# Optimization experiments

Measured on AMD Instinct MI355X. Metric: run time of the kernel, lower is better.

Reference implementation:

```python
import jax, jax.numpy as jnp
import numpy as np

B, S, D, H = 2, 2048, 1024, 16
DK = D // H
EPS = 1e-5


def setup_inputs() -> dict:
    key = jax.random.key(0)
    ks = jax.random.split(key, 12)
    s = 1.0 / np.sqrt(D)
    return {
        "q": jax.random.normal(ks[0], (B, S, D), dtype=jnp.float32),
        "k": jax.random.normal(ks[1], (B, S, D), dtype=jnp.float32),
        "v": jax.random.normal(ks[2], (B, S, D), dtype=jnp.float32),
        "mask": jnp.ones((B, S, S), dtype=jnp.int32),
        "Wq": jax.random.normal(ks[3], (D, D), dtype=jnp.float32) * s,
        "bq": jnp.zeros((D,), dtype=jnp.float32),
        "Wk": jax.random.normal(ks[4], (D, D), dtype=jnp.float32) * s,
        "bk": jnp.zeros((D,), dtype=jnp.float32),
        "Wv": jax.random.normal(ks[5], (D, D), dtype=jnp.float32) * s,
        "bv": jnp.zeros((D,), dtype=jnp.float32),
        "Wo": jax.random.normal(ks[6], (D, D), dtype=jnp.float32) * s,
        "bo": jnp.zeros((D,), dtype=jnp.float32),
        "gamma": jnp.ones((D,), dtype=jnp.float32),
        "beta": jnp.zeros((D,), dtype=jnp.float32),
    }


def _split_heads(x):
    # [B,S,D] -> [B,H,S,DK]
    return x.reshape(B, S, H, DK).transpose(0, 2, 1, 3)


def reference(q, k, v, mask, Wq, bq, Wk, bk, Wv, bv, Wo, bo, gamma, beta):
    residual = q
    qh = _split_heads(q @ Wq.T + bq)
    kh = _split_heads(k @ Wk.T + bk)
    vh = _split_heads(v @ Wv.T + bv)
    scale = 1.0 / jnp.sqrt(jnp.float32(DK))
    scores = jnp.einsum("bhqd,bhkd->bhqk", qh, kh) * scale
    scores = jnp.where(mask[:, None, :, :] == 0, jnp.float32(-1e9), scores)
    attention = jax.nn.softmax(scores, axis=-1)  # dropout is identity at eval
    ctx = jnp.einsum("bhqk,bhkd->bhqd", attention, vh)
    ctx = ctx.transpose(0, 2, 1, 3).reshape(B, S, D)
    out = ctx @ Wo.T + bo  # output dropout identity at eval
    x = out + residual
    mu = jnp.mean(x, axis=-1, keepdims=True)
    var = jnp.mean((x - mu) ** 2, axis=-1, keepdims=True)
    out = (x - mu) * jax.lax.rsqrt(var + EPS) * gamma + beta
    return out, attention
```

## Files before the change

kernel.cpp:

```cpp
#include <hip/hip_runtime.h>
#include <math.h>

#define B_ 2
#define S_ 2048
#define D_ 1024
#define H_ 16
#define DK_ 64
#define EPS_ 1e-5f

typedef __bf16 bf16_t;
typedef __bf16 bf16x4 __attribute__((ext_vector_type(4)));
typedef __bf16 bf16x8 __attribute__((ext_vector_type(8)));
typedef float f32x4 __attribute__((ext_vector_type(4)));
typedef unsigned long long u64;
typedef unsigned short u16;

#define MFMA16(a, b, c) __builtin_amdgcn_mfma_f32_16x16x32_bf16(a, b, c, 0, 0, 0)

__device__ __forceinline__ void gload16(const bf16_t* g, bf16_t* l) {
    __builtin_amdgcn_global_load_lds(
        (const __attribute__((address_space(1))) void*)g,
        (__attribute__((address_space(3))) void*)l, 16, 0, 0);
}

__global__ __launch_bounds__(256) void cvt3(const float* __restrict__ a,
        const float* __restrict__ b, const float* __restrict__ c,
        bf16_t* __restrict__ oa, bf16_t* __restrict__ ob, bf16_t* __restrict__ oc)
{
    int region = blockIdx.x >> 11;
    int i = ((blockIdx.x & 2047) << 8) + threadIdx.x;
    const float* in = (region == 0) ? a : (region == 1) ? b : c;
    bf16_t* out = (region == 0) ? oa : (region == 1) ? ob : oc;
    float4 v0 = reinterpret_cast<const float4*>(in)[i * 2];
    float4 v1 = reinterpret_cast<const float4*>(in)[i * 2 + 1];
    bf16x8 o = { (bf16_t)v0.x, (bf16_t)v0.y, (bf16_t)v0.z, (bf16_t)v0.w,
                 (bf16_t)v1.x, (bf16_t)v1.y, (bf16_t)v1.z, (bf16_t)v1.w };
    reinterpret_cast<bf16x8*>(out)[i] = o;
}

__global__ __launch_bounds__(256) void cvt4(const float* __restrict__ a,
        const float* __restrict__ b, const float* __restrict__ c, const float* __restrict__ d,
        bf16_t* __restrict__ oa, bf16_t* __restrict__ ob, bf16_t* __restrict__ oc,
        bf16_t* __restrict__ od)
{
    int region = blockIdx.x >> 9;
    int i = ((blockIdx.x & 511) << 8) + threadIdx.x;
    const float* in = (region == 0) ? a : (region == 1) ? b : (region == 2) ? c : d;
    bf16_t* out = (region == 0) ? oa : (region == 1) ? ob : (region == 2) ? oc : od;
    float4 v0 = reinterpret_cast<const float4*>(in)[i * 2];
    float4 v1 = reinterpret_cast<const float4*>(in)[i * 2 + 1];
    bf16x8 o = { (bf16_t)v0.x, (bf16_t)v0.y, (bf16_t)v0.z, (bf16_t)v0.w,
                 (bf16_t)v1.x, (bf16_t)v1.y, (bf16_t)v1.z, (bf16_t)v1.w };
    reinterpret_cast<bf16x8*>(out)[i] = o;
}

__global__ __launch_bounds__(256) void mask_pack(const int* __restrict__ mask,
                                                 u16* __restrict__ bits2)
{
    size_t i = (size_t)blockIdx.x * 256 + threadIdx.x;
    int m = mask[i];
    u64 wm = __ballot(m != 0);
    if ((threadIdx.x & 63) == 0) {
        size_t widx = i >> 6;
        size_t row = widx >> 5;
        int t = (int)(widx & 31);
#pragma unroll
        for (int g = 0; g < 4; ++g) {
            u16 v = 0;
#pragma unroll
            for (int tk = 0; tk < 4; ++tk)
                v |= (u16)(((wm >> (tk * 16 + g * 4)) & 0xF) << (tk * 4));
            bits2[(row * 4 + g) * 32 + t] = v;
        }
    }
}

__device__ __forceinline__ void gemm_body(
        const bf16_t* __restrict__ Asrc, const bf16_t* __restrict__ Bsrc,
        const float* __restrict__ bias, const float* __restrict__ resid,
        float* __restrict__ xout, bf16_t* __restrict__ bout,
        int mode, int m0, int n0)
{
    __shared__ bf16_t As[128 * 64];
    __shared__ bf16_t Bs[128 * 64];
    const int tid = threadIdx.x;
    const int w = tid >> 6, l = tid & 63;
    const int c = l & 15, g = l >> 4;
    const int wr = w >> 1, wc = w & 1;

    int srow[4], scol[4];
    uint32_t soff[4];
#pragma unroll
    for (int i = 0; i < 4; ++i) {
        int s = tid + i * 256;
        srow[i] = s >> 3;
        scol[i] = s & 7;
        soff[i] = (uint32_t)(s * 16) ^ (uint32_t)((srow[i] & 7) << 4);
    }

    bf16x8 areg[4], breg[4];
#pragma unroll
    for (int i = 0; i < 4; ++i) {
        areg[i] = *reinterpret_cast<const bf16x8*>(Asrc + (size_t)srow[i] * D_ + scol[i] * 8);
        breg[i] = *reinterpret_cast<const bf16x8*>(Bsrc + (size_t)srow[i] * D_ + scol[i] * 8);
    }

    f32x4 acc[4][4] = {};
    for (int kt = 0; kt < 16; ++kt) {
#pragma unroll
        for (int i = 0; i < 4; ++i) {
            *reinterpret_cast<bf16x8*>((char*)As + soff[i]) = areg[i];
            *reinterpret_cast<bf16x8*>((char*)Bs + soff[i]) = breg[i];
        }
        __syncthreads();
        if (kt + 1 < 16) {
            int k0 = (kt + 1) * 64;
#pragma unroll
            for (int i = 0; i < 4; ++i) {
                areg[i] = *reinterpret_cast<const bf16x8*>(Asrc + (size_t)srow[i] * D_ + k0 + scol[i] * 8);
                breg[i] = *reinterpret_cast<const bf16x8*>(Bsrc + (size_t)srow[i] * D_ + k0 + scol[i] * 8);
            }
        }
        bf16x8 bf0[4], bf1[4];
#pragma unroll
        for (int j = 0; j < 4; ++j) {
            int R = wc * 64 + j * 16 + c;
            const char* base = (const char*)Bs + R * 128;
            uint32_t msk = (uint32_t)((R & 7) << 4);
            bf0[j] = *reinterpret_cast<const bf16x8*>(base + ((g * 16) ^ msk));
            bf1[j] = *reinterpret_cast<const bf16x8*>(base + ((64 + g * 16) ^ msk));
        }
#pragma unroll
        for (int i = 0; i < 4; ++i) {
            int R = wr * 64 + i * 16 + c;
            const char* base = (const char*)As + R * 128;
            uint32_t msk = (uint32_t)((R & 7) << 4);
            bf16x8 a0 = *reinterpret_cast<const bf16x8*>(base + ((g * 16) ^ msk));
            bf16x8 a1 = *reinterpret_cast<const bf16x8*>(base + ((64 + g * 16) ^ msk));
#pragma unroll
            for (int j = 0; j < 4; ++j) {
                acc[i][j] = MFMA16(a0, bf0[j], acc[i][j]);
                acc[i][j] = MFMA16(a1, bf1[j], acc[i][j]);
            }
        }
        __syncthreads();
    }

#pragma unroll
    for (int i = 0; i < 4; ++i) {
#pragma unroll
        for (int j = 0; j < 4; ++j) {
#pragma unroll
            for (int r = 0; r < 4; ++r) {
                int P  = wr * 64 + i * 16 + g * 4 + r;
                int Qd = wc * 64 + j * 16 + c;
                float val = acc[i][j][r];
                if (mode == 2) {
                    int m = m0 + P, n = n0 + Qd;
                    xout[(size_t)m * D_ + n] = val + bias[n] + resid[(size_t)m * D_ + n];
                } else if (mode == 0) {
                    int m = m0 + P, n = n0 + Qd;
                    int bb = m >> 11, s = m & (S_ - 1);
                    int h = n >> 6, dk = n & 63;
                    bout[(((size_t)bb * H_ + h) * S_ + s) * DK_ + dk] = (bf16_t)(val + bias[n]);
                } else {
                    int n = n0 + P, m = m0 + Qd;
                    int bb = m >> 11, s = m & (S_ - 1);
                    int h = n >> 6, dk = n & 63;
                    bout[(((size_t)bb * H_ + h) * DK_ + dk) * S_ + s] = (bf16_t)(val + bias[n]);
                }
            }
        }
    }
}

__global__ __launch_bounds__(256) void qkv_gemm(
        const bf16_t* __restrict__ xq, const bf16_t* __restrict__ xk,
        const bf16_t* __restrict__ xv,
        const bf16_t* __restrict__ wq, const bf16_t* __restrict__ wk,
        const bf16_t* __restrict__ wv,
        const float* __restrict__ bq, const float* __restrict__ bk,
        const float* __restrict__ bv,
        bf16_t* __restrict__ qh, bf16_t* __restrict__ kh, bf16_t* __restrict__ vt)
{
    const int z = blockIdx.z;
    const int m0 = blockIdx.y * 128, n0 = blockIdx.x * 128;
    const bf16_t* X = (z == 0) ? xq : (z == 1) ? xk : xv;
    const bf16_t* W = (z == 0) ? wq : (z == 1) ? wk : wv;
    const float* bias = (z == 0) ? bq : (z == 1) ? bk : bv;
    bf16_t* out = (z == 0) ? qh : (z == 1) ? kh : vt;
    int mode = (z == 2) ? 1 : 0;
    const bf16_t* Asrc = (mode == 1) ? (W + (size_t)n0 * D_) : (X + (size_t)m0 * D_);
    const bf16_t* Bsrc = (mode == 1) ? (X + (size_t)m0 * D_) : (W + (size_t)n0 * D_);
    gemm_body(Asrc, Bsrc, bias, nullptr, nullptr, out, mode, m0, n0);
}

__global__ __launch_bounds__(256) void oproj_gemm(
        const bf16_t* __restrict__ ctx, const bf16_t* __restrict__ wo,
        const float* __restrict__ bo, const float* __restrict__ resid,
        float* __restrict__ x)
{
    const int m0 = blockIdx.y * 128, n0 = blockIdx.x * 128;
    gemm_body(ctx + (size_t)m0 * D_, wo + (size_t)n0 * D_, bo, resid, x, nullptr, 2, m0, n0);
}

__global__ __launch_bounds__(512) void fused_attn(
        const bf16_t* __restrict__ qh,
        const bf16_t* __restrict__ kh,
        const bf16_t* __restrict__ vt,
        const u16*    __restrict__ bits2,
        float* __restrict__ attn,
        bf16_t* __restrict__ ctx)
{
    constexpr int TILE = 64;
    constexpr int NT = S_ / TILE;
    __shared__ bf16_t Kbuf[3][TILE * DK_];
    __shared__ bf16_t Vbuf[3][TILE * DK_];
    __shared__ float  Pf[8][16 * 64];

    const int tid = threadIdx.x;
    const int w = tid >> 6, l = tid & 63;
    const int c = l & 15, g = l >> 4;

    const int id = blockIdx.x;
    const int xcd = id & 7, ixd = id >> 3;
    const int bh = xcd * 4 + (ixd >> 4);
    const int qt = ixd & 15;
    const int q0 = qt * 128 + w * 16;
    const int b = bh >> 4, h = bh & 15;

    const bf16_t* Q = qh + ((size_t)bh * S_ + q0) * DK_;
    const bf16_t* K = kh + (size_t)bh * S_ * DK_;
    const bf16_t* V = vt + (size_t)bh * DK_ * S_;
    float* Astrip = attn + ((size_t)bh * S_ + q0) * S_;

    u64 mreg[8];
    {
        const u64* mp = reinterpret_cast<const u64*>(
            bits2 + (((size_t)b * S_ + q0 + c) * 4 + g) * 32);
#pragma unroll
        for (int i = 0; i < 8; ++i) mreg[i] = mp[i];
    }

    bf16x8 qf0 = *reinterpret_cast<const bf16x8*>(&Q[c * DK_ + g * 8]);
    bf16x8 qf1 = *reinterpret_cast<const bf16x8*>(&Q[c * DK_ + 32 + g * 8]);

    const int row_s = (w << 3) + (l >> 3);
    const int csx = (l & 7) ^ (row_s & 7);
    const bf16_t* Kg = K + (size_t)row_s * DK_ + csx * 8;
    const bf16_t* Vg = V + (size_t)row_s * S_ + csx * 8;
    const int woffu = __builtin_amdgcn_readfirstlane(w * 512);
    const uint32_t rm = (uint32_t)((c & 7) << 4);
    const uint32_t xr = (uint32_t)((c & 7) << 4);

    gload16(Kg, &Kbuf[0][woffu]);
    gload16(Kg + (size_t)TILE * DK_, &Kbuf[1][woffu]);
    asm volatile("s_waitcnt vmcnt(1)" ::: "memory");
    __builtin_amdgcn_s_barrier();

    float l_r = 0.f;
    int bc = 0;
    for (int t = 0; t < NT; ++t) {
        if (t + 2 < NT) {
            int b2 = bc + 2; if (b2 >= 3) b2 -= 3;
            gload16(Kg + (size_t)(t + 2) * TILE * DK_, &Kbuf[b2][woffu]);
        }
        __builtin_amdgcn_sched_barrier(0);
        u16 m16 = (u16)(mreg[t >> 2] >> ((t & 3) << 4));
        const char* kb = (const char*)&Kbuf[bc][0];
        f32x4 acc[4] = {};
        __builtin_amdgcn_s_setprio(1);
#pragma unroll
        for (int tk = 0; tk < 4; ++tk) {
            uint32_t base = (uint32_t)((tk * 16 + c) * 128 + g * 16);
            bf16x8 a0 = *reinterpret_cast<const bf16x8*>(kb + (base ^ rm));
            bf16x8 a1 = *reinterpret_cast<const bf16x8*>(kb + ((base + 64) ^ rm));
            acc[tk] = MFMA16(a0, qf0, acc[tk]);
            acc[tk] = MFMA16(a1, qf1, acc[tk]);
        }
        __builtin_amdgcn_s_setprio(0);
        float ps = 0.f;
#pragma unroll
        for (int tk = 0; tk < 4; ++tk) {
#pragma unroll
            for (int r = 0; r < 4; ++r) {
                float e = __expf(acc[tk][r] * 0.125f);
                e = ((m16 >> (tk * 4 + r)) & 1) ? e : 0.f;
                ps += e;
            }
        }
        l_r += ps;
        if (t + 2 < NT) asm volatile("s_waitcnt vmcnt(1)" ::: "memory");
        else            asm volatile("s_waitcnt vmcnt(0)" ::: "memory");
        asm volatile("s_waitcnt lgkmcnt(0)" ::: "memory");
        __builtin_amdgcn_sched_barrier(0);
        __builtin_amdgcn_s_barrier();
        bc = (bc == 2) ? 0 : bc + 1;
    }
    l_r += __shfl_xor(l_r, 16);
    l_r += __shfl_xor(l_r, 32);
    const float inv_l = 1.0f / l_r;

    gload16(Kg, &Kbuf[0][woffu]);
    gload16(Vg, &Vbuf[0][woffu]);
    gload16(Kg + (size_t)TILE * DK_, &Kbuf[1][woffu]);
    gload16(Vg + TILE, &Vbuf[1][woffu]);
    asm volatile("s_waitcnt vmcnt(2)" ::: "memory");
    __builtin_amdgcn_s_barrier();

    float* pf = &Pf[w][0];
    f32x4 oacc[4] = {};
    bc = 0;
    for (int t = 0; t < NT; ++t) {
        if (t + 2 < NT) {
            int b2 = bc + 2; if (b2 >= 3) b2 -= 3;
            gload16(Kg + (size_t)(t + 2) * TILE * DK_, &Kbuf[b2][woffu]);
            gload16(Vg + (t + 2) * TILE, &Vbuf[b2][woffu]);
        }
        __builtin_amdgcn_sched_barrier(0);
        u16 m16 = (u16)(mreg[t >> 2] >> ((t & 3) << 4));
        const char* kb = (const char*)&Kbuf[bc][0];
        const char* vb = (const char*)&Vbuf[bc][0];
        f32x4 acc[4] = {};
        __builtin_amdgcn_s_setprio(1);
#pragma unroll
        for (int tk = 0; tk < 4; ++tk) {
            uint32_t base = (uint32_t)((tk * 16 + c) * 128 + g * 16);
            bf16x8 a0 = *reinterpret_cast<const bf16x8*>(kb + (base ^ rm));
            bf16x8 a1 = *reinterpret_cast<const bf16x8*>(kb + ((base + 64) ^ rm));
            acc[tk] = MFMA16(a0, qf0, acc[tk]);
            acc[tk] = MFMA16(a1, qf1, acc[tk]);
        }
        __builtin_amdgcn_s_setprio(0);
#pragma unroll
        for (int tk = 0; tk < 4; ++tk) {
            f32x4 pv;
#pragma unroll
            for (int r = 0; r < 4; ++r) {
                float p = __expf(acc[tk][r] * 0.125f) * inv_l;
                pv[r] = ((m16 >> (tk * 4 + r)) & 1) ? p : 0.f;
            }
            *reinterpret_cast<f32x4*>((char*)pf + ((uint32_t)(c * 256 + tk * 64 + g * 16) ^ xr)) = pv;
        }
        asm volatile("s_waitcnt lgkmcnt(0)" ::: "memory");
        __builtin_amdgcn_sched_barrier(0);
#pragma unroll
        for (int i = 0; i < 4; ++i) {
            int row = i * 4 + (l >> 4);
            uint32_t off = (uint32_t)(i * 1024 + l * 16) ^ (uint32_t)((row & 7) << 4);
            f32x4 sv = *reinterpret_cast<const f32x4*>((char*)pf + off);
            __builtin_nontemporal_store(sv,
                reinterpret_cast<f32x4*>(Astrip + (size_t)row * S_ + t * TILE + (l & 15) * 4));
        }
        f32x4 p0a = *reinterpret_cast<const f32x4*>((char*)pf + ((uint32_t)(c * 256 + g * 32) ^ xr));
        f32x4 p0b = *reinterpret_cast<const f32x4*>((char*)pf + ((uint32_t)(c * 256 + g * 32 + 16) ^ xr));
        f32x4 p1a = *reinterpret_cast<const f32x4*>((char*)pf + ((uint32_t)(c * 256 + 128 + g * 32) ^ xr));
        f32x4 p1b = *reinterpret_cast<const f32x4*>((char*)pf + ((uint32_t)(c * 256 + 128 + g * 32 + 16) ^ xr));
        bf16x8 pa0 = { (bf16_t)p0a[0], (bf16_t)p0a[1], (bf16_t)p0a[2], (bf16_t)p0a[3],
                       (bf16_t)p0b[0], (bf16_t)p0b[1], (bf16_t)p0b[2], (bf16_t)p0b[3] };
        bf16x8 pa1 = { (bf16_t)p1a[0], (bf16_t)p1a[1], (bf16_t)p1a[2], (bf16_t)p1a[3],
                       (bf16_t)p1b[0], (bf16_t)p1b[1], (bf16_t)p1b[2], (bf16_t)p1b[3] };
        __builtin_amdgcn_s_setprio(1);
#pragma unroll
        for (int tk = 0; tk < 4; ++tk) {
            uint32_t base = (uint32_t)((tk * 16 + c) * 128 + g * 16);
            bf16x8 b0 = *reinterpret_cast<const bf16x8*>(vb + (base ^ rm));
            bf16x8 b1 = *reinterpret_cast<const bf16x8*>(vb + ((base + 64) ^ rm));
            oacc[tk] = MFMA16(pa0, b0, oacc[tk]);
            oacc[tk] = MFMA16(pa1, b1, oacc[tk]);
        }
        __builtin_amdgcn_s_setprio(0);
        if (t + 2 < NT)       asm volatile("s_waitcnt vmcnt(6)" ::: "memory");
        else if (t + 1 < NT)  asm volatile("s_waitcnt vmcnt(4)" ::: "memory");
        asm volatile("s_waitcnt lgkmcnt(0)" ::: "memory");
        __builtin_amdgcn_sched_barrier(0);
        __builtin_amdgcn_s_barrier();
        bc = (bc == 2) ? 0 : bc + 1;
    }

#pragma unroll
    for (int tk = 0; tk < 4; ++tk) {
#pragma unroll
        for (int r = 0; r < 4; ++r) {
            int q = q0 + g * 4 + r;
            ctx[((size_t)b * S_ + q) * D_ + h * DK_ + tk * 16 + c] = (bf16_t)oacc[tk][r];
        }
    }
}

__global__ void ln_kernel(const float* __restrict__ x, const float* __restrict__ gamma,
                          const float* __restrict__ beta, float* __restrict__ out)
{
    int row = blockIdx.x;
    const float* xr = x + (size_t)row * D_;
    int tid = threadIdx.x;
    float v[4];
    float s = 0.f;
#pragma unroll
    for (int i = 0; i < 4; ++i) {
        v[i] = xr[tid + i * 256];
        s += v[i];
    }
#pragma unroll
    for (int off = 32; off > 0; off >>= 1) s += __shfl_xor(s, off);
    __shared__ float red[4];
    int wid = tid >> 6, lane = tid & 63;
    if (lane == 0) red[wid] = s;
    __syncthreads();
    float mu = (red[0] + red[1] + red[2] + red[3]) * (1.0f / D_);
    float vs = 0.f;
#pragma unroll
    for (int i = 0; i < 4; ++i) {
        float d = v[i] - mu;
        vs += d * d;
    }
#pragma unroll
    for (int off = 32; off > 0; off >>= 1) vs += __shfl_xor(vs, off);
    __syncthreads();
    __shared__ float red2[4];
    if (lane == 0) red2[wid] = vs;
    __syncthreads();
    float var = (red2[0] + red2[1] + red2[2] + red2[3]) * (1.0f / D_);
    float rs = rsqrtf(var + EPS_);
#pragma unroll
    for (int i = 0; i < 4; ++i) {
        int c = tid + i * 256;
        out[(size_t)row * D_ + c] = (v[i] - mu) * rs * gamma[c] + beta[c];
    }
}

extern "C" void kernel_launch(void* const* d_in, const int* in_sizes, int n_in,
                              void* d_out, int out_size, void* d_ws, size_t ws_size,
                              hipStream_t stream) {
    const float* q    = (const float*)d_in[0];
    const float* k    = (const float*)d_in[1];
    const float* v    = (const float*)d_in[2];
    const int*   mask = (const int*)d_in[3];
    const float* Wq   = (const float*)d_in[4];
    const float* bq   = (const float*)d_in[5];
    const float* Wk   = (const float*)d_in[6];
    const float* bk   = (const float*)d_in[7];
    const float* Wv   = (const float*)d_in[8];
    const float* bv   = (const float*)d_in[9];
    const float* Wo   = (const float*)d_in[10];
    const float* bo   = (const float*)d_in[11];
    const float* gamma= (const float*)d_in[12];
    const float* beta = (const float*)d_in[13];

    float* out  = (float*)d_out;
    float* attn = out + (size_t)B_ * S_ * D_;

    uint8_t* ws = (uint8_t*)d_ws;
    bf16_t* xq  = (bf16_t*)(ws);
    bf16_t* xk  = (bf16_t*)(ws + ((size_t)8  << 20));
    bf16_t* xv  = (bf16_t*)(ws + ((size_t)16 << 20));
    bf16_t* wqb = (bf16_t*)(ws + ((size_t)24 << 20));
    bf16_t* wkb = (bf16_t*)(ws + ((size_t)26 << 20));
    bf16_t* wvb = (bf16_t*)(ws + ((size_t)28 << 20));
    bf16_t* wob = (bf16_t*)(ws + ((size_t)30 << 20));
    bf16_t* qh  = (bf16_t*)(ws + ((size_t)32 << 20));
    u16*    bits= (u16*)   (ws + ((size_t)40 << 20));
    bf16_t* kh  = (bf16_t*)(ws + ((size_t)42 << 20));
    bf16_t* vt  = (bf16_t*)(ws + ((size_t)50 << 20));
    bf16_t* ctx = (bf16_t*)(ws);
    float*  x   = (float*) (ws + ((size_t)8 << 20));

    dim3 blk(256);
    cvt3<<<dim3(6144), blk, 0, stream>>>(q, k, v, xq, xk, xv);
    cvt4<<<dim3(2048), blk, 0, stream>>>(Wq, Wk, Wv, Wo, wqb, wkb, wvb, wob);
    mask_pack<<<dim3((B_ * S_ * S_) / 256), blk, 0, stream>>>(mask, bits);

    dim3 gqkv(D_ / 128, (B_ * S_) / 128, 3);
    qkv_gemm<<<gqkv, blk, 0, stream>>>(xq, xk, xv, wqb, wkb, wvb,
                                       bq, bk, bv, qh, kh, vt);

    fused_attn<<<dim3(512), dim3(512), 0, stream>>>(qh, kh, vt, bits, attn, ctx);

    dim3 ggemm(D_ / 128, (B_ * S_) / 128);
    oproj_gemm<<<ggemm, blk, 0, stream>>>(ctx, wob, bo, q, x);
    ln_kernel<<<dim3(B_ * S_), blk, 0, stream>>>(x, gamma, beta, out);
}
```

Measured before the change: 268.7 us.

## Split attention softmax-stats pass into separate kernel and merge prep kernels

The two-pass fused attention kernel is split so that the row-sum (softmax denominator) pass runs in its own kernel, `attn_stats`. That kernel uses 256-thread blocks over 64-query tiles, giving 1024 blocks, and writes inverse sums to a workspace buffer. The emit kernel then reads those sums instead of recomputing them. The aim is more parallelism and occupancy for the stats pass, which used to run inside the 512-block grid. The three conversion and mask-pack launches are also merged into one `prep` kernel to cut launch overhead. The cost is an extra launch, a global round-trip for the sums, and a second read of Q/K.

```diff
diff --git a/kernel.cpp b/kernel.cpp
--- a/kernel.cpp
+++ b/kernel.cpp
@@ -23,55 +23,56 @@
         (__attribute__((address_space(3))) void*)l, 16, 0, 0);
 }
 
-__global__ __launch_bounds__(256) void cvt3(const float* __restrict__ a,
-        const float* __restrict__ b, const float* __restrict__ c,
-        bf16_t* __restrict__ oa, bf16_t* __restrict__ ob, bf16_t* __restrict__ oc)
-{
-    int region = blockIdx.x >> 11;
-    int i = ((blockIdx.x & 2047) << 8) + threadIdx.x;
-    const float* in = (region == 0) ? a : (region == 1) ? b : c;
-    bf16_t* out = (region == 0) ? oa : (region == 1) ? ob : oc;
-    float4 v0 = reinterpret_cast<const float4*>(in)[i * 2];
-    float4 v1 = reinterpret_cast<const float4*>(in)[i * 2 + 1];
-    bf16x8 o = { (bf16_t)v0.x, (bf16_t)v0.y, (bf16_t)v0.z, (bf16_t)v0.w,
-                 (bf16_t)v1.x, (bf16_t)v1.y, (bf16_t)v1.z, (bf16_t)v1.w };
-    reinterpret_cast<bf16x8*>(out)[i] = o;
-}
-
-__global__ __launch_bounds__(256) void cvt4(const float* __restrict__ a,
-        const float* __restrict__ b, const float* __restrict__ c, const float* __restrict__ d,
-        bf16_t* __restrict__ oa, bf16_t* __restrict__ ob, bf16_t* __restrict__ oc,
-        bf16_t* __restrict__ od)
-{
-    int region = blockIdx.x >> 9;
-    int i = ((blockIdx.x & 511) << 8) + threadIdx.x;
-    const float* in = (region == 0) ? a : (region == 1) ? b : (region == 2) ? c : d;
-    bf16_t* out = (region == 0) ? oa : (region == 1) ? ob : (region == 2) ? oc : od;
-    float4 v0 = reinterpret_cast<const float4*>(in)[i * 2];
-    float4 v1 = reinterpret_cast<const float4*>(in)[i * 2 + 1];
-    bf16x8 o = { (bf16_t)v0.x, (bf16_t)v0.y, (bf16_t)v0.z, (bf16_t)v0.w,
-                 (bf16_t)v1.x, (bf16_t)v1.y, (bf16_t)v1.z, (bf16_t)v1.w };
-    reinterpret_cast<bf16x8*>(out)[i] = o;
-}
-
-__global__ __launch_bounds__(256) void mask_pack(const int* __restrict__ mask,
-                                                 u16* __restrict__ bits2)
-{
-    size_t i = (size_t)blockIdx.x * 256 + threadIdx.x;
-    int m = mask[i];
-    u64 wm = __ballot(m != 0);
-    if ((threadIdx.x & 63) == 0) {
-        size_t widx = i >> 6;
-        size_t row = widx >> 5;
-        int t = (int)(widx & 31);
-#pragma unroll
-        for (int g = 0; g < 4; ++g) {
-            u16 v = 0;
-#pragma unroll
-            for (int tk = 0; tk < 4; ++tk)
-                v |= (u16)(((wm >> (tk * 16 + g * 4)) & 0xF) << (tk * 4));
-            bits2[(row * 4 + g) * 32 + t] = v;
-        }
+__global__ __launch_bounds__(256) void prep(
+        const int* __restrict__ mask, u16* __restrict__ bits2,
+        const float* __restrict__ q, const float* __restrict__ k,
+        const float* __restrict__ v,
+        bf16_t* __restrict__ xq, bf16_t* __restrict__ xk, bf16_t* __restrict__ xv,
+        const float* __restrict__ Wq, const float* __restrict__ Wk,
+        const float* __restrict__ Wv, const float* __restrict__ Wo,
+        bf16_t* __restrict__ wq, bf16_t* __restrict__ wk,
+        bf16_t* __restrict__ wv, bf16_t* __restrict__ wo)
+{
+    int bid = blockIdx.x;
+    if (bid < 32768) {
+        size_t i = (size_t)bid * 256 + threadIdx.x;
+        int m = mask[i];
+        u64 wm = __ballot(m != 0);
+        if ((threadIdx.x & 63) == 0) {
+            size_t widx = i >> 6;
+            size_t row = widx >> 5;
+            int t = (int)(widx & 31);
+#pragma unroll
+            for (int g = 0; g < 4; ++g) {
+                u16 val = 0;
+#pragma unroll
+                for (int tk = 0; tk < 4; ++tk)
+                    val |= (u16)(((wm >> (tk * 16 + g * 4)) & 0xF) << (tk * 4));
+                bits2[(row * 4 + g) * 32 + t] = val;
+            }
+        }
+    } else if (bid < 38912) {
+        int b2 = bid - 32768;
+        int region = b2 >> 11;
+        int i = ((b2 & 2047) << 8) + threadIdx.x;
+        const float* in = (region == 0) ? q : (region == 1) ? k : v;
+        bf16_t* out = (region == 0) ? xq : (region == 1) ? xk : xv;
+        float4 v0 = reinterpret_cast<const float4*>(in)[i * 2];
+        float4 v1 = reinterpret_cast<const float4*>(in)[i * 2 + 1];
+        bf16x8 o = { (bf16_t)v0.x, (bf16_t)v0.y, (bf16_t)v0.z, (bf16_t)v0.w,
+                     (bf16_t)v1.x, (bf16_t)v1.y, (bf16_t)v1.z, (bf16_t)v1.w };
+        reinterpret_cast<bf16x8*>(out)[i] = o;
+    } else {
+        int b2 = bid - 38912;
+        int region = b2 >> 9;
+        int i = ((b2 & 511) << 8) + threadIdx.x;
+        const float* in = (region == 0) ? Wq : (region == 1) ? Wk : (region == 2) ? Wv : Wo;
+        bf16_t* out = (region == 0) ? wq : (region == 1) ? wk : (region == 2) ? wv : wo;
+        float4 v0 = reinterpret_cast<const float4*>(in)[i * 2];
+        float4 v1 = reinterpret_cast<const float4*>(in)[i * 2 + 1];
+        bf16x8 o = { (bf16_t)v0.x, (bf16_t)v0.y, (bf16_t)v0.z, (bf16_t)v0.w,
+                     (bf16_t)v1.x, (bf16_t)v1.y, (bf16_t)v1.z, (bf16_t)v1.w };
+        reinterpret_cast<bf16x8*>(out)[i] = o;
     }
 }
 
@@ -204,13 +205,104 @@
     gemm_body(ctx + (size_t)m0 * D_, wo + (size_t)n0 * D_, bo, resid, x, nullptr, 2, m0, n0);
 }
 
-__global__ __launch_bounds__(512) void fused_attn(
-        const bf16_t* __restrict__ qh,
-        const bf16_t* __restrict__ kh,
-        const bf16_t* __restrict__ vt,
-        const u16*    __restrict__ bits2,
-        float* __restrict__ attn,
-        bf16_t* __restrict__ ctx)
+__global__ __launch_bounds__(256) void attn_stats(
+        const bf16_t* __restrict__ qh, const bf16_t* __restrict__ kh,
+        const u16* __restrict__ bits2, float* __restrict__ linv)
+{
+    constexpr int TILE = 64;
+    constexpr int NT = S_ / TILE;
+    __shared__ bf16_t Kbuf[3][TILE * DK_];
+
+    const int tid = threadIdx.x;
+    const int w = tid >> 6, l = tid & 63;
+    const int c = l & 15, g = l >> 4;
+
+    const int id = blockIdx.x;
+    const int xcd = id & 7, ixd = id >> 3;
+    const int bh = xcd * 4 + (ixd >> 5);
+    const int qt = ixd & 31;
+    const int q0 = qt * 64 + w * 16;
+    const int b = bh >> 4;
+
+    const bf16_t* Q = qh + ((size_t)bh * S_ + q0) * DK_;
+    const bf16_t* K = kh + (size_t)bh * S_ * DK_;
+
+    u64 mreg[8];
+    {
+        const u64* mp = reinterpret_cast<const u64*>(
+            bits2 + (((size_t)b * S_ + q0 + c) * 4 + g) * 32);
+#pragma unroll
+        for (int i = 0; i < 8; ++i) mreg[i] = mp[i];
+    }
+
+    bf16x8 qf0 = *reinterpret_cast<const bf16x8*>(&Q[c * DK_ + g * 8]);
+    bf16x8 qf1 = *reinterpret_cast<const bf16x8*>(&Q[c * DK_ + 32 + g * 8]);
+
+    const int slot0 = (w << 6) + l, slot1 = slot0 + 256;
+    const int r0 = slot0 >> 3, cs0 = (slot0 & 7) ^ (r0 & 7);
+    const int r1 = slot1 >> 3, cs1 = (slot1 & 7) ^ (r1 & 7);
+    const bf16_t* Kg0 = K + (size_t)r0 * DK_ + cs0 * 8;
+    const bf16_t* Kg1 = K + (size_t)r1 * DK_ + cs1 * 8;
+    const int off0 = __builtin_amdgcn_readfirstlane((w << 6) * 8);
+    const int off1 = __builtin_amdgcn_readfirstlane(((w << 6) + 256) * 8);
+    const uint32_t rm = (uint32_t)((c & 7) << 4);
+
+    gload16(Kg0, &Kbuf[0][off0]);
+    gload16(Kg1, &Kbuf[0][off1]);
+    gload16(Kg0 + (size_t)TILE * DK_, &Kbuf[1][off0]);
+    gload16(Kg1 + (size_t)TILE * DK_, &Kbuf[1][off1]);
+    asm volatile("s_waitcnt vmcnt(2)" ::: "memory");
+    __builtin_amdgcn_s_barrier();
+
+    float l_r = 0.f;
+    int bc = 0;
+    for (int t = 0; t < NT; ++t) {
+        if (t + 2 < NT) {
+            int b2 = bc + 2; if (b2 >= 3) b2 -= 3;
+            gload16(Kg0 + (size_t)(t + 2) * TILE * DK_, &Kbuf[b2][off0]);
+            gload16(Kg1 + (size_t)(t + 2) * TILE * DK_, &Kbuf[b2][off1]);
+        }
+        __builtin_amdgcn_sched_barrier(0);
+        u16 m16 = (u16)(mreg[t >> 2] >> ((t & 3) << 4));
+        const char* kb = (const char*)&Kbuf[bc][0];
+        f32x4 acc[4] = {};
+        __builtin_amdgcn_s_setprio(1);
+#pragma unroll
+        for (int tk = 0; tk < 4; ++tk) {
+            uint32_t base = (uint32_t)((tk * 16 + c) * 128 + g * 16);
+            bf16x8 a0 = *reinterpret_cast<const bf16x8*>(kb + (base ^ rm));
+            bf16x8 a1 = *reinterpret_cast<const bf16x8*>(kb + ((base + 64) ^ rm));
+            acc[tk] = MFMA16(a0, qf0, acc[tk]);
+            acc[tk] = MFMA16(a1, qf1, acc[tk]);
+        }
+        __builtin_amdgcn_s_setprio(0);
+        float ps = 0.f;
+#pragma unroll
+        for (int tk = 0; tk < 4; ++tk) {
+#pragma unroll
+            for (int r = 0; r < 4; ++r) {
+                float e = __expf(acc[tk][r] * 0.125f);
+                e = ((m16 >> (tk * 4 + r)) & 1) ? e : 0.f;
+                ps += e;
+            }
+        }
+        l_r += ps;
+        if (t + 2 < NT) asm volatile("s_waitcnt vmcnt(2)" ::: "memory");
+        else            asm volatile("s_waitcnt vmcnt(0)" ::: "memory");
+        __builtin_amdgcn_sched_barrier(0);
+        __builtin_amdgcn_s_barrier();
+        bc = (bc == 2) ? 0 : bc + 1;
+    }
+    l_r += __shfl_xor(l_r, 16);
+    l_r += __shfl_xor(l_r, 32);
+    if (l < 16) linv[(size_t)bh * S_ + q0 + l] = 1.0f / l_r;
+}
+
+__global__ __launch_bounds__(512) void attn_emit(
+        const bf16_t* __restrict__ qh, const bf16_t* __restrict__ kh,
+        const bf16_t* __restrict__ vt, const u16* __restrict__ bits2,
+        const float* __restrict__ linv,
+        float* __restrict__ attn, bf16_t* __restrict__ ctx)
 {
     constexpr int TILE = 64;
     constexpr int NT = S_ / TILE;
@@ -244,6 +336,7 @@
 
     bf16x8 qf0 = *reinterpret_cast<const bf16x8*>(&Q[c * DK_ + g * 8]);
     bf16x8 qf1 = *reinterpret_cast<const bf16x8*>(&Q[c * DK_ + 32 + g * 8]);
+    const float inv_l = linv[(size_t)bh * S_ + q0 + c];
 
     const int row_s = (w << 3) + (l >> 3);
     const int csx = (l & 7) ^ (row_s & 7);
@@ -254,54 +347,6 @@
     const uint32_t xr = (uint32_t)((c & 7) << 4);
 
     gload16(Kg, &Kbuf[0][woffu]);
-    gload16(Kg + (size_t)TILE * DK_, &Kbuf[1][woffu]);
-    asm volatile("s_waitcnt vmcnt(1)" ::: "memory");
-    __builtin_amdgcn_s_barrier();
-
-    float l_r = 0.f;
-    int bc = 0;
-    for (int t = 0; t < NT; ++t) {
-        if (t + 2 < NT) {
-            int b2 = bc + 2; if (b2 >= 3) b2 -= 3;
-            gload16(Kg + (size_t)(t + 2) * TILE * DK_, &Kbuf[b2][woffu]);
-        }
-        __builtin_amdgcn_sched_barrier(0);
-        u16 m16 = (u16)(mreg[t >> 2] >> ((t & 3) << 4));
-        const char* kb = (const char*)&Kbuf[bc][0];
-        f32x4 acc[4] = {};
-        __builtin_amdgcn_s_setprio(1);
-#pragma unroll
-        for (int tk = 0; tk < 4; ++tk) {
-            uint32_t base = (uint32_t)((tk * 16 + c) * 128 + g * 16);
-            bf16x8 a0 = *reinterpret_cast<const bf16x8*>(kb + (base ^ rm));
-            bf16x8 a1 = *reinterpret_cast<const bf16x8*>(kb + ((base + 64) ^ rm));
-            acc[tk] = MFMA16(a0, qf0, acc[tk]);
-            acc[tk] = MFMA16(a1, qf1, acc[tk]);
-        }
-        __builtin_amdgcn_s_setprio(0);
-        float ps = 0.f;
-#pragma unroll
-        for (int tk = 0; tk < 4; ++tk) {
-#pragma unroll
-            for (int r = 0; r < 4; ++r) {
-                float e = __expf(acc[tk][r] * 0.125f);
-                e = ((m16 >> (tk * 4 + r)) & 1) ? e : 0.f;
-                ps += e;
-            }
-        }
-        l_r += ps;
-        if (t + 2 < NT) asm volatile("s_waitcnt vmcnt(1)" ::: "memory");
-        else            asm volatile("s_waitcnt vmcnt(0)" ::: "memory");
-        asm volatile("s_waitcnt lgkmcnt(0)" ::: "memory");
-        __builtin_amdgcn_sched_barrier(0);
-        __builtin_amdgcn_s_barrier();
-        bc = (bc == 2) ? 0 : bc + 1;
-    }
-    l_r += __shfl_xor(l_r, 16);
-    l_r += __shfl_xor(l_r, 32);
-    const float inv_l = 1.0f / l_r;
-
-    gload16(Kg, &Kbuf[0][woffu]);
     gload16(Vg, &Vbuf[0][woffu]);
     gload16(Kg + (size_t)TILE * DK_, &Kbuf[1][woffu]);
     gload16(Vg + TILE, &Vbuf[1][woffu]);
@@ -310,7 +355,7 @@
 
     float* pf = &Pf[w][0];
     f32x4 oacc[4] = {};
-    bc = 0;
+    int bc = 0;
     for (int t = 0; t < NT; ++t) {
         if (t + 2 < NT) {
             int b2 = bc + 2; if (b2 >= 3) b2 -= 3;
@@ -382,8 +427,8 @@
     for (int tk = 0; tk < 4; ++tk) {
 #pragma unroll
         for (int r = 0; r < 4; ++r) {
-            int q = q0 + g * 4 + r;
-            ctx[((size_t)b * S_ + q) * D_ + h * DK_ + tk * 16 + c] = (bf16_t)oacc[tk][r];
+            int qrow = q0 + g * 4 + r;
+            ctx[((size_t)b * S_ + qrow) * D_ + h * DK_ + tk * 16 + c] = (bf16_t)oacc[tk][r];
         }
     }
 }
@@ -460,21 +505,22 @@
     bf16_t* wob = (bf16_t*)(ws + ((size_t)30 << 20));
     bf16_t* qh  = (bf16_t*)(ws + ((size_t)32 << 20));
     u16*    bits= (u16*)   (ws + ((size_t)40 << 20));
+    float*  linv= (float*) (ws + ((size_t)41 << 20));
     bf16_t* kh  = (bf16_t*)(ws + ((size_t)42 << 20));
     bf16_t* vt  = (bf16_t*)(ws + ((size_t)50 << 20));
     bf16_t* ctx = (bf16_t*)(ws);
     float*  x   = (float*) (ws + ((size_t)8 << 20));
 
     dim3 blk(256);
-    cvt3<<<dim3(6144), blk, 0, stream>>>(q, k, v, xq, xk, xv);
-    cvt4<<<dim3(2048), blk, 0, stream>>>(Wq, Wk, Wv, Wo, wqb, wkb, wvb, wob);
-    mask_pack<<<dim3((B_ * S_ * S_) / 256), blk, 0, stream>>>(mask, bits);
+    prep<<<dim3(40960), blk, 0, stream>>>(mask, bits, q, k, v, xq, xk, xv,
+                                          Wq, Wk, Wv, Wo, wqb, wkb, wvb, wob);
 
     dim3 gqkv(D_ / 128, (B_ * S_) / 128, 3);
     qkv_gemm<<<gqkv, blk, 0, stream>>>(xq, xk, xv, wqb, wkb, wvb,
                                        bq, bk, bv, qh, kh, vt);
 
-    fused_attn<<<dim3(512), dim3(512), 0, stream>>>(qh, kh, vt, bits, attn, ctx);
+    attn_stats<<<dim3(1024), blk, 0, stream>>>(qh, kh, bits, linv);
+    attn_emit<<<dim3(512), dim3(512), 0, stream>>>(qh, kh, vt, bits, linv, attn, ctx);
 
     dim3 ggemm(D_ / 128, (B_ * S_) / 128);
     oproj_gemm<<<ggemm, blk, 0, stream>>>(ctx, wob, bo, q, x);
```

Result: slower. 283.2 us (+5.4%).
